# Optimization experiments

Measured on AMD Instinct MI355X. Metric: run time of the kernel, lower is better.

Reference implementation:

```python
import jax, jax.numpy as jnp
import numpy as np

B, C = 4096, 10000
TAU = 1.0
MIN_K, MAX_K = 30, 100


def setup_inputs() -> dict:
    key = jax.random.key(0)
    k1, k2 = jax.random.split(key, 2)
    logit = jax.random.normal(k1, (B, C), dtype=jnp.float32)
    target = jax.random.randint(k2, (B,), 0, C)
    # long-tailed class counts: exponential decay from 1000 down to 5
    cls_num = np.exp(np.linspace(np.log(1000.0), np.log(5.0), C)).astype(np.float32)
    cls_num_ratio = cls_num / cls_num.sum()
    log_cls_num = jnp.asarray(np.log(cls_num_ratio + 1e-6), dtype=jnp.float32)
    freq = (cls_num.max() / cls_num).astype(np.float32)
    freq_norm = (freq - freq.min()) / (freq.max() - freq.min() + 1e-6)
    k_per_class = jnp.asarray((freq_norm * (MAX_K - MIN_K) + MIN_K).astype(np.int32))
    return {"logit": logit, "target": target, "log_cls_num": log_cls_num,
            "k_per_class": k_per_class}


def reference(logit, target, log_cls_num, k_per_class):
    b, c = logit.shape
    rows = jnp.arange(b)
    # logit-adjusted cross entropy (loss_full)
    logit_adj = logit + TAU * log_cls_num[None, :]
    log_p_adj = jax.nn.log_softmax(logit_adj, axis=1)  # [B, C]
    loss_full = -jnp.mean(log_p_adj[rows, target])
    # per-row variable-k top-k mask on the ORIGINAL logits
    prob_adj = jnp.exp(log_p_adj)
    k = jnp.minimum(k_per_class[target], c)            # [B]
    sorted_desc = -jnp.sort(-logit, axis=1)            # [B, C] descending
    thresh = sorted_desc[rows, k - 1]                  # k-th largest per row
    mask = logit >= thresh[:, None]
    masked_prob = jnp.where(mask, prob_adj, 0.0) + 1e-6
    masked_prob = masked_prob / masked_prob.sum(axis=1, keepdims=True)
    loss_topk = -jnp.mean(jnp.log(masked_prob)[rows, target])
    return 0.5 * loss_full + 0.5 * loss_topk
```

## Files before the change

kernel.cpp:

```cpp
#include <hip/hip_runtime.h>

#define BLOCK 256
#define C_DIM 10000
#define C4 (C_DIM / 4)
#define NIT ((C4 + BLOCK - 1) / BLOCK)
#define TAU 1.0f
#define CAP 2048
#define PIV_HI 2.0f
#define PIV_LO 1.0f

__device__ __forceinline__ unsigned flip_key(float f) {
    unsigned u = __float_as_uint(f);
    return (u & 0x80000000u) ? ~u : (u | 0x80000000u);
}
__device__ __forceinline__ float unflip_key(unsigned k) {
    unsigned u = (k & 0x80000000u) ? (k & 0x7fffffffu) : ~k;
    return __uint_as_float(u);
}

__global__ void zero_out_kernel(float* out, int n) {
    int i = blockIdx.x * blockDim.x + threadIdx.x;
    if (i < n) out[i] = 0.f;
}

__device__ __forceinline__ void scan_pick(unsigned* hist, int shift, int tid,
                                          unsigned* shp, unsigned* shkr, unsigned* shcnt) {
    unsigned h0 = hist[4 * tid + 0], h1 = hist[4 * tid + 1];
    unsigned h2 = hist[4 * tid + 2], h3 = hist[4 * tid + 3];
    unsigned loc = h0 + h1 + h2 + h3;
    unsigned suf = loc;
    for (int off = 1; off < 64; off <<= 1) {
        unsigned o = __shfl_down(suf, off);
        if (tid + off < 64) suf += o;
    }
    unsigned sufex = suf - loc;
    unsigned kr = *shkr;
    unsigned s3 = sufex + h3;
    unsigned s2 = s3 + h2;
    unsigned s1 = s2 + h1;
    unsigned s0 = s1 + h0;
    int bsel = -1; unsigned newkr = 0, newcnt = 0;
    if      (s3 >= kr && s3 - h3 < kr) { bsel = 4 * tid + 3; newkr = kr - (s3 - h3); newcnt = h3; }
    else if (s2 >= kr && s2 - h2 < kr) { bsel = 4 * tid + 2; newkr = kr - (s2 - h2); newcnt = h2; }
    else if (s1 >= kr && s1 - h1 < kr) { bsel = 4 * tid + 1; newkr = kr - (s1 - h1); newcnt = h1; }
    else if (s0 >= kr && s0 - h0 < kr) { bsel = 4 * tid + 0; newkr = kr - (s0 - h0); newcnt = h0; }
    if (bsel >= 0) {
        *shp |= ((unsigned)bsel << shift);
        *shkr = newkr;
        *shcnt = newcnt;
    }
}

__global__ __launch_bounds__(BLOCK, 8) void topk_la_loss_kernel(
    const float* __restrict__ logit, const int* __restrict__ target,
    const float* __restrict__ lcn, const int* __restrict__ kpc,
    float* __restrict__ out, int B) {
    __shared__ unsigned hist[256];
    __shared__ unsigned candk[CAP];
    __shared__ unsigned short candi[CAP];
    __shared__ float red_a[4], red_b[4];
    __shared__ unsigned sh_nc, sh_prefix, sh_kr, sh_cnt;
    __shared__ int sh_path, sh_k;
    __shared__ float sh_thresh, sh_madj;

    const int row = blockIdx.x;
    const int tid = threadIdx.x;
    const int lane = tid & 63;
    const int wid = tid >> 6;
    const float* lrow = logit + (size_t)row * C_DIM;

    if (tid == 0) {
        int t = target[row];
        int k = kpc[t];
        if (k > C_DIM) k = C_DIM;
        sh_k = k;
        sh_nc = 0u;
    }
    __syncthreads();

    float z = 0.f, madj = -INFINITY;
    for (int it = 0; it < NIT; ++it) {
        int j4 = it * BLOCK + tid;
        if (j4 < C4) {
            float4 f = ((const float4*)lrow)[j4];
            float4 l = ((const float4*)lcn)[j4];
            float a0 = f.x + TAU * l.x, a1 = f.y + TAU * l.y;
            float a2 = f.z + TAU * l.z, a3 = f.w + TAU * l.w;
            z += __expf(a0) + __expf(a1) + __expf(a2) + __expf(a3);
            madj = fmaxf(madj, fmaxf(fmaxf(a0, a1), fmaxf(a2, a3)));
            int j = 4 * j4;
            if (f.x >= PIV_HI) { unsigned i = atomicAdd(&sh_nc, 1u); if (i < CAP) { candk[i] = __float_as_uint(f.x); candi[i] = (unsigned short)(j + 0); } }
            if (f.y >= PIV_HI) { unsigned i = atomicAdd(&sh_nc, 1u); if (i < CAP) { candk[i] = __float_as_uint(f.y); candi[i] = (unsigned short)(j + 1); } }
            if (f.z >= PIV_HI) { unsigned i = atomicAdd(&sh_nc, 1u); if (i < CAP) { candk[i] = __float_as_uint(f.z); candi[i] = (unsigned short)(j + 2); } }
            if (f.w >= PIV_HI) { unsigned i = atomicAdd(&sh_nc, 1u); if (i < CAP) { candk[i] = __float_as_uint(f.w); candi[i] = (unsigned short)(j + 3); } }
        }
    }
    for (int off = 32; off; off >>= 1) madj = fmaxf(madj, __shfl_down(madj, off));
    if (lane == 0) red_a[wid] = madj;
    __syncthreads();

    if (tid == 0) {
        sh_madj = fmaxf(fmaxf(red_a[0], red_a[1]), fmaxf(red_a[2], red_a[3]));
        unsigned n = sh_nc;
        unsigned k = (unsigned)sh_k;
        sh_path = (n >= k && n <= CAP) ? 0 : ((n < k) ? 1 : 2);
        sh_kr = k;
        sh_prefix = 0u;
        sh_cnt = n;
    }
    __syncthreads();

    if (sh_path == 1) {
        if (tid == 0) sh_nc = 0u;
        __syncthreads();
        for (int it = 0; it < NIT; ++it) {
            int j4 = it * BLOCK + tid;
            if (j4 < C4) {
                float4 f = ((const float4*)lrow)[j4];
                int j = 4 * j4;
                if (f.x >= PIV_LO) { unsigned i = atomicAdd(&sh_nc, 1u); if (i < CAP) { candk[i] = __float_as_uint(f.x); candi[i] = (unsigned short)(j + 0); } }
                if (f.y >= PIV_LO) { unsigned i = atomicAdd(&sh_nc, 1u); if (i < CAP) { candk[i] = __float_as_uint(f.y); candi[i] = (unsigned short)(j + 1); } }
                if (f.z >= PIV_LO) { unsigned i = atomicAdd(&sh_nc, 1u); if (i < CAP) { candk[i] = __float_as_uint(f.z); candi[i] = (unsigned short)(j + 2); } }
                if (f.w >= PIV_LO) { unsigned i = atomicAdd(&sh_nc, 1u); if (i < CAP) { candk[i] = __float_as_uint(f.w); candi[i] = (unsigned short)(j + 3); } }
            }
        }
        __syncthreads();
        if (tid == 0) {
            unsigned n = sh_nc;
            unsigned k = (unsigned)sh_k;
            sh_path = (n >= k && n <= CAP) ? 0 : 2;
            sh_kr = k;
            sh_prefix = 0u;
            sh_cnt = n;
        }
        __syncthreads();
    }

    const int path = sh_path;
    const float madjB = sh_madj;

    if (path == 0) {
        const int nc = (int)sh_cnt;
        unsigned kmask = 0u;
        for (int q = 0; q < 4; ++q) {
            if (sh_cnt == 1u) break;
            const int shift = 24 - 8 * q;
            hist[tid] = 0u;
            __syncthreads();
            const unsigned pref = sh_prefix;
            for (int i = tid; i < nc; i += BLOCK) {
                unsigned kk = candk[i];
                if ((kk & kmask) == pref) atomicAdd(&hist[(kk >> shift) & 0xFFu], 1u);
            }
            __syncthreads();
            if (tid < 64) scan_pick(hist, shift, tid, &sh_prefix, &sh_kr, &sh_cnt);
            kmask |= (0xFFu << shift);
            __syncthreads();
        }
        if (sh_cnt == 1u && kmask != 0xFFFFFFFFu) {
            const unsigned pref = sh_prefix;
            __syncthreads();
            for (int i = tid; i < nc; i += BLOCK) {
                unsigned kk = candk[i];
                if ((kk & kmask) == pref) sh_prefix = kk;
            }
            __syncthreads();
        }
        if (tid == 0) sh_thresh = __uint_as_float(sh_prefix);
    } else {
        for (int p = 0; p < 4; ++p) {
            const int shift = 24 - 8 * p;
            const unsigned pmask = p ? (0xFFFFFFFFu << (shift + 8)) : 0u;
            hist[tid] = 0u;
            __syncthreads();
            const unsigned pref = sh_prefix;
            for (int it = 0; it < NIT; ++it) {
                int j4 = it * BLOCK + tid;
                if (j4 < C4) {
                    float4 f = ((const float4*)lrow)[j4];
                    unsigned kk;
                    kk = flip_key(f.x); if ((kk & pmask) == pref) atomicAdd(&hist[(kk >> shift) & 0xFFu], 1u);
                    kk = flip_key(f.y); if ((kk & pmask) == pref) atomicAdd(&hist[(kk >> shift) & 0xFFu], 1u);
                    kk = flip_key(f.z); if ((kk & pmask) == pref) atomicAdd(&hist[(kk >> shift) & 0xFFu], 1u);
                    kk = flip_key(f.w); if ((kk & pmask) == pref) atomicAdd(&hist[(kk >> shift) & 0xFFu], 1u);
                }
            }
            __syncthreads();
            if (tid < 64) scan_pick(hist, shift, tid, &sh_prefix, &sh_kr, &sh_cnt);
            __syncthreads();
        }
        if (tid == 0) sh_thresh = unflip_key(sh_prefix);
    }
    __syncthreads();

    const float thresh = sh_thresh;
    const bool rare = fabsf(madjB) > 80.f;

    float sm = 0.f;
    if (!rare) {
        if (path == 0) {
            const int nc = (int)((sh_nc <= CAP) ? sh_nc : CAP);
            for (int i = tid; i < nc; i += BLOCK) {
                unsigned kk = candk[i];
                float v = __uint_as_float(kk);
                if (v >= thresh) sm += __expf(v + TAU * lcn[candi[i]]);
            }
        } else {
            for (int it = 0; it < NIT; ++it) {
                int j4 = it * BLOCK + tid;
                if (j4 < C4) {
                    float4 f = ((const float4*)lrow)[j4];
                    float4 l = ((const float4*)lcn)[j4];
                    if (f.x >= thresh) sm += __expf(f.x + TAU * l.x);
                    if (f.y >= thresh) sm += __expf(f.y + TAU * l.y);
                    if (f.z >= thresh) sm += __expf(f.z + TAU * l.z);
                    if (f.w >= thresh) sm += __expf(f.w + TAU * l.w);
                }
            }
        }
    } else {
        z = 0.f;
        for (int it = 0; it < NIT; ++it) {
            int j4 = it * BLOCK + tid;
            if (j4 < C4) {
                float4 f = ((const float4*)lrow)[j4];
                float4 l = ((const float4*)lcn)[j4];
                float e;
                e = __expf(f.x + TAU * l.x - madjB); z += e; if (f.x >= thresh) sm += e;
                e = __expf(f.y + TAU * l.y - madjB); z += e; if (f.y >= thresh) sm += e;
                e = __expf(f.z + TAU * l.z - madjB); z += e; if (f.z >= thresh) sm += e;
                e = __expf(f.w + TAU * l.w - madjB); z += e; if (f.w >= thresh) sm += e;
            }
        }
    }

    for (int off = 32; off; off >>= 1) {
        z  += __shfl_down(z, off);
        sm += __shfl_down(sm, off);
    }
    if (lane == 0) { red_a[wid] = z; red_b[wid] = sm; }
    __syncthreads();

    if (tid == 0) {
        float Z = red_a[0] + red_a[1] + red_a[2] + red_a[3];
        float S = red_b[0] + red_b[1] + red_b[2] + red_b[3];
        int t = target[row];
        float logit_t = lrow[t];
        float adj_t = logit_t + TAU * lcn[t];
        float sub = rare ? madjB : 0.f;
        float lpt = adj_t - sub - __logf(Z);
        float p_num = ((logit_t >= thresh) ? __expf(lpt) : 0.f) + 1e-6f;
        float Smask = S / Z + (float)C_DIM * 1e-6f;
        float loss = 0.5f * (-lpt + __logf(Smask) - __logf(p_num));
        atomicAdd(out, loss / (float)B);
    }
}

extern "C" void kernel_launch(void* const* d_in, const int* in_sizes, int n_in,
                              void* d_out, int out_size, void* d_ws, size_t ws_size,
                              hipStream_t stream) {
    const float* logit  = (const float*)d_in[0];
    const int*   target = (const int*)d_in[1];
    const float* lcn    = (const float*)d_in[2];
    const int*   kpc    = (const int*)d_in[3];
    float* out = (float*)d_out;
    const int B = in_sizes[1];

    zero_out_kernel<<<1, 64, 0, stream>>>(out, out_size);
    topk_la_loss_kernel<<<B, BLOCK, 0, stream>>>(logit, target, lcn, kpc, out, B);
}
```

Baseline: 270.5 us.

## Process one row per wavefront with ballot-based candidate compaction

Each 64-lane wavefront now handles a whole row, with four rows per block, instead of one row per 256-thread block. Block-wide __syncthreads and shared-memory reductions are replaced by wave shuffles, and the radix pick is done inside the wave. Shared atomic counters for candidate gathering give way to ballot/mbcnt prefix compaction, and the candidate buffer shrinks to 512 entries per wave. Each lane now walks more of the row, so per-row latency goes up. The smaller candidate cap also sends more rows to the full-row radix fallback when more than 512 values pass the pivot.

```diff
diff --git a/kernel.cpp b/kernel.cpp
--- a/kernel.cpp
+++ b/kernel.cpp
@@ -1,11 +1,12 @@
 #include <hip/hip_runtime.h>
 
 #define BLOCK 256
+#define WPB 4
 #define C_DIM 10000
 #define C4 (C_DIM / 4)
-#define NIT ((C4 + BLOCK - 1) / BLOCK)
+#define NIT4 ((C4 + 63) / 64)
 #define TAU 1.0f
-#define CAP 2048
+#define CAP 512
 #define PIV_HI 2.0f
 #define PIV_LO 1.0f
 
@@ -17,197 +18,190 @@
     unsigned u = (k & 0x80000000u) ? (k & 0x7fffffffu) : ~k;
     return __uint_as_float(u);
 }
+__device__ __forceinline__ int mbcnt64(unsigned long long m) {
+    return (int)__builtin_amdgcn_mbcnt_hi((unsigned)(m >> 32),
+               __builtin_amdgcn_mbcnt_lo((unsigned)(m & 0xffffffffu), 0u));
+}
 
 __global__ void zero_out_kernel(float* out, int n) {
     int i = blockIdx.x * blockDim.x + threadIdx.x;
     if (i < n) out[i] = 0.f;
 }
 
-__device__ __forceinline__ void scan_pick(unsigned* hist, int shift, int tid,
-                                          unsigned* shp, unsigned* shkr, unsigned* shcnt) {
-    unsigned h0 = hist[4 * tid + 0], h1 = hist[4 * tid + 1];
-    unsigned h2 = hist[4 * tid + 2], h3 = hist[4 * tid + 3];
-    unsigned loc = h0 + h1 + h2 + h3;
+__device__ __forceinline__ void wave_pick(uint4 hv, int lane, int shift,
+                                          unsigned& prefix, unsigned& kr, unsigned& cnt) {
+    unsigned loc = hv.x + hv.y + hv.z + hv.w;
     unsigned suf = loc;
+    #pragma unroll
     for (int off = 1; off < 64; off <<= 1) {
-        unsigned o = __shfl_down(suf, off);
-        if (tid + off < 64) suf += o;
+        unsigned o = (unsigned)__shfl_down((int)suf, off);
+        if (lane + off < 64) suf += o;
     }
     unsigned sufex = suf - loc;
-    unsigned kr = *shkr;
-    unsigned s3 = sufex + h3;
-    unsigned s2 = s3 + h2;
-    unsigned s1 = s2 + h1;
-    unsigned s0 = s1 + h0;
-    int bsel = -1; unsigned newkr = 0, newcnt = 0;
-    if      (s3 >= kr && s3 - h3 < kr) { bsel = 4 * tid + 3; newkr = kr - (s3 - h3); newcnt = h3; }
-    else if (s2 >= kr && s2 - h2 < kr) { bsel = 4 * tid + 2; newkr = kr - (s2 - h2); newcnt = h2; }
-    else if (s1 >= kr && s1 - h1 < kr) { bsel = 4 * tid + 1; newkr = kr - (s1 - h1); newcnt = h1; }
-    else if (s0 >= kr && s0 - h0 < kr) { bsel = 4 * tid + 0; newkr = kr - (s0 - h0); newcnt = h0; }
-    if (bsel >= 0) {
-        *shp |= ((unsigned)bsel << shift);
-        *shkr = newkr;
-        *shcnt = newcnt;
-    }
-}
-
-__global__ __launch_bounds__(BLOCK, 8) void topk_la_loss_kernel(
+    unsigned s3 = sufex + hv.w;
+    unsigned s2 = s3 + hv.z;
+    unsigned s1 = s2 + hv.y;
+    unsigned s0 = s1 + hv.x;
+    int bsel = -1; unsigned nkr = 0u, ncnt = 0u;
+    if      (s3 >= kr && s3 - hv.w < kr) { bsel = 4 * lane + 3; nkr = kr - (s3 - hv.w); ncnt = hv.w; }
+    else if (s2 >= kr && s2 - hv.z < kr) { bsel = 4 * lane + 2; nkr = kr - (s2 - hv.z); ncnt = hv.z; }
+    else if (s1 >= kr && s1 - hv.y < kr) { bsel = 4 * lane + 1; nkr = kr - (s1 - hv.y); ncnt = hv.y; }
+    else if (s0 >= kr && s0 - hv.x < kr) { bsel = 4 * lane + 0; nkr = kr - (s0 - hv.x); ncnt = hv.x; }
+    unsigned long long pm = __ballot(bsel >= 0);
+    int src = __ffsll((unsigned long long)pm) - 1;
+    prefix |= ((unsigned)__shfl(bsel, src)) << shift;
+    kr  = (unsigned)__shfl((int)nkr, src);
+    cnt = (unsigned)__shfl((int)ncnt, src);
+}
+
+__global__ __launch_bounds__(BLOCK, 4) void topk_la_loss_kernel(
     const float* __restrict__ logit, const int* __restrict__ target,
     const float* __restrict__ lcn, const int* __restrict__ kpc,
     float* __restrict__ out, int B) {
-    __shared__ unsigned hist[256];
-    __shared__ unsigned candk[CAP];
-    __shared__ unsigned short candi[CAP];
-    __shared__ float red_a[4], red_b[4];
-    __shared__ unsigned sh_nc, sh_prefix, sh_kr, sh_cnt;
-    __shared__ int sh_path, sh_k;
-    __shared__ float sh_thresh, sh_madj;
-
-    const int row = blockIdx.x;
+    __shared__ unsigned candk[WPB][CAP];
+    __shared__ unsigned short candi[WPB][CAP];
+    __shared__ unsigned hist[WPB][256];
+
     const int tid = threadIdx.x;
     const int lane = tid & 63;
     const int wid = tid >> 6;
+    const int row = blockIdx.x * WPB + wid;
+    if (row >= B) return;
+
     const float* lrow = logit + (size_t)row * C_DIM;
-
-    if (tid == 0) {
-        int t = target[row];
-        int k = kpc[t];
-        if (k > C_DIM) k = C_DIM;
-        sh_k = k;
-        sh_nc = 0u;
-    }
-    __syncthreads();
-
-    float z = 0.f, madj = -INFINITY;
-    for (int it = 0; it < NIT; ++it) {
-        int j4 = it * BLOCK + tid;
+    unsigned* ck = candk[wid];
+    unsigned short* ci = candi[wid];
+    unsigned* h = hist[wid];
+
+    const int t = target[row];
+    int k = kpc[t]; if (k > C_DIM) k = C_DIM;
+
+    float z = 0.f, madj = -__builtin_inff();
+    unsigned nb = 0u;
+    #pragma unroll 2
+    for (int it = 0; it < NIT4; ++it) {
+        const int j4 = it * 64 + lane;
+        float4 f, l;
         if (j4 < C4) {
-            float4 f = ((const float4*)lrow)[j4];
-            float4 l = ((const float4*)lcn)[j4];
-            float a0 = f.x + TAU * l.x, a1 = f.y + TAU * l.y;
-            float a2 = f.z + TAU * l.z, a3 = f.w + TAU * l.w;
-            z += __expf(a0) + __expf(a1) + __expf(a2) + __expf(a3);
-            madj = fmaxf(madj, fmaxf(fmaxf(a0, a1), fmaxf(a2, a3)));
-            int j = 4 * j4;
-            if (f.x >= PIV_HI) { unsigned i = atomicAdd(&sh_nc, 1u); if (i < CAP) { candk[i] = __float_as_uint(f.x); candi[i] = (unsigned short)(j + 0); } }
-            if (f.y >= PIV_HI) { unsigned i = atomicAdd(&sh_nc, 1u); if (i < CAP) { candk[i] = __float_as_uint(f.y); candi[i] = (unsigned short)(j + 1); } }
-            if (f.z >= PIV_HI) { unsigned i = atomicAdd(&sh_nc, 1u); if (i < CAP) { candk[i] = __float_as_uint(f.z); candi[i] = (unsigned short)(j + 2); } }
-            if (f.w >= PIV_HI) { unsigned i = atomicAdd(&sh_nc, 1u); if (i < CAP) { candk[i] = __float_as_uint(f.w); candi[i] = (unsigned short)(j + 3); } }
-        }
-    }
-    for (int off = 32; off; off >>= 1) madj = fmaxf(madj, __shfl_down(madj, off));
-    if (lane == 0) red_a[wid] = madj;
-    __syncthreads();
-
-    if (tid == 0) {
-        sh_madj = fmaxf(fmaxf(red_a[0], red_a[1]), fmaxf(red_a[2], red_a[3]));
-        unsigned n = sh_nc;
-        unsigned k = (unsigned)sh_k;
-        sh_path = (n >= k && n <= CAP) ? 0 : ((n < k) ? 1 : 2);
-        sh_kr = k;
-        sh_prefix = 0u;
-        sh_cnt = n;
-    }
-    __syncthreads();
-
-    if (sh_path == 1) {
-        if (tid == 0) sh_nc = 0u;
-        __syncthreads();
-        for (int it = 0; it < NIT; ++it) {
-            int j4 = it * BLOCK + tid;
-            if (j4 < C4) {
-                float4 f = ((const float4*)lrow)[j4];
-                int j = 4 * j4;
-                if (f.x >= PIV_LO) { unsigned i = atomicAdd(&sh_nc, 1u); if (i < CAP) { candk[i] = __float_as_uint(f.x); candi[i] = (unsigned short)(j + 0); } }
-                if (f.y >= PIV_LO) { unsigned i = atomicAdd(&sh_nc, 1u); if (i < CAP) { candk[i] = __float_as_uint(f.y); candi[i] = (unsigned short)(j + 1); } }
-                if (f.z >= PIV_LO) { unsigned i = atomicAdd(&sh_nc, 1u); if (i < CAP) { candk[i] = __float_as_uint(f.z); candi[i] = (unsigned short)(j + 2); } }
-                if (f.w >= PIV_LO) { unsigned i = atomicAdd(&sh_nc, 1u); if (i < CAP) { candk[i] = __float_as_uint(f.w); candi[i] = (unsigned short)(j + 3); } }
-            }
-        }
-        __syncthreads();
-        if (tid == 0) {
-            unsigned n = sh_nc;
-            unsigned k = (unsigned)sh_k;
-            sh_path = (n >= k && n <= CAP) ? 0 : 2;
-            sh_kr = k;
-            sh_prefix = 0u;
-            sh_cnt = n;
-        }
-        __syncthreads();
-    }
-
-    const int path = sh_path;
-    const float madjB = sh_madj;
-
+            f = ((const float4*)lrow)[j4];
+            l = ((const float4*)lcn)[j4];
+        } else {
+            f = make_float4(-1e30f, -1e30f, -1e30f, -1e30f);
+            l = make_float4(0.f, 0.f, 0.f, 0.f);
+        }
+        const float a0 = f.x + TAU * l.x, a1 = f.y + TAU * l.y;
+        const float a2 = f.z + TAU * l.z, a3 = f.w + TAU * l.w;
+        z += __expf(a0) + __expf(a1) + __expf(a2) + __expf(a3);
+        madj = fmaxf(madj, fmaxf(fmaxf(a0, a1), fmaxf(a2, a3)));
+        const int j = 4 * j4;
+        unsigned long long m;
+        m = __ballot(f.x >= PIV_HI);
+        if (f.x >= PIV_HI) { unsigned p = nb + (unsigned)mbcnt64(m); if (p < CAP) { ck[p] = __float_as_uint(f.x); ci[p] = (unsigned short)(j + 0); } }
+        nb += (unsigned)__popcll(m);
+        m = __ballot(f.y >= PIV_HI);
+        if (f.y >= PIV_HI) { unsigned p = nb + (unsigned)mbcnt64(m); if (p < CAP) { ck[p] = __float_as_uint(f.y); ci[p] = (unsigned short)(j + 1); } }
+        nb += (unsigned)__popcll(m);
+        m = __ballot(f.z >= PIV_HI);
+        if (f.z >= PIV_HI) { unsigned p = nb + (unsigned)mbcnt64(m); if (p < CAP) { ck[p] = __float_as_uint(f.z); ci[p] = (unsigned short)(j + 2); } }
+        nb += (unsigned)__popcll(m);
+        m = __ballot(f.w >= PIV_HI);
+        if (f.w >= PIV_HI) { unsigned p = nb + (unsigned)mbcnt64(m); if (p < CAP) { ck[p] = __float_as_uint(f.w); ci[p] = (unsigned short)(j + 3); } }
+        nb += (unsigned)__popcll(m);
+    }
+    #pragma unroll
+    for (int off = 32; off; off >>= 1) madj = fmaxf(madj, __shfl_xor(madj, off));
+
+    unsigned n = nb;
+    int path = (n >= (unsigned)k && n <= CAP) ? 0 : ((n < (unsigned)k) ? 1 : 2);
+
+    if (path == 1) {
+        nb = 0u;
+        for (int it = 0; it < NIT4; ++it) {
+            const int j4 = it * 64 + lane;
+            float4 f;
+            if (j4 < C4) f = ((const float4*)lrow)[j4];
+            else f = make_float4(-1e30f, -1e30f, -1e30f, -1e30f);
+            const int j = 4 * j4;
+            unsigned long long m;
+            m = __ballot(f.x >= PIV_LO);
+            if (f.x >= PIV_LO) { unsigned p = nb + (unsigned)mbcnt64(m); if (p < CAP) { ck[p] = __float_as_uint(f.x); ci[p] = (unsigned short)(j + 0); } }
+            nb += (unsigned)__popcll(m);
+            m = __ballot(f.y >= PIV_LO);
+            if (f.y >= PIV_LO) { unsigned p = nb + (unsigned)mbcnt64(m); if (p < CAP) { ck[p] = __float_as_uint(f.y); ci[p] = (unsigned short)(j + 1); } }
+            nb += (unsigned)__popcll(m);
+            m = __ballot(f.z >= PIV_LO);
+            if (f.z >= PIV_LO) { unsigned p = nb + (unsigned)mbcnt64(m); if (p < CAP) { ck[p] = __float_as_uint(f.z); ci[p] = (unsigned short)(j + 2); } }
+            nb += (unsigned)__popcll(m);
+            m = __ballot(f.w >= PIV_LO);
+            if (f.w >= PIV_LO) { unsigned p = nb + (unsigned)mbcnt64(m); if (p < CAP) { ck[p] = __float_as_uint(f.w); ci[p] = (unsigned short)(j + 3); } }
+            nb += (unsigned)__popcll(m);
+        }
+        n = nb;
+        path = (n >= (unsigned)k && n <= CAP) ? 0 : 2;
+    }
+
+    float thresh;
     if (path == 0) {
-        const int nc = (int)sh_cnt;
-        unsigned kmask = 0u;
+        const int nc = (int)n;
+        unsigned prefix = 0u, kr = (unsigned)k, cnt = n, kmask = 0u;
         for (int q = 0; q < 4; ++q) {
-            if (sh_cnt == 1u) break;
+            if (cnt == 1u) break;
             const int shift = 24 - 8 * q;
-            hist[tid] = 0u;
-            __syncthreads();
-            const unsigned pref = sh_prefix;
-            for (int i = tid; i < nc; i += BLOCK) {
-                unsigned kk = candk[i];
-                if ((kk & kmask) == pref) atomicAdd(&hist[(kk >> shift) & 0xFFu], 1u);
-            }
-            __syncthreads();
-            if (tid < 64) scan_pick(hist, shift, tid, &sh_prefix, &sh_kr, &sh_cnt);
+            *(uint4*)&h[4 * lane] = make_uint4(0u, 0u, 0u, 0u);
+            for (int i = lane; i < nc; i += 64) {
+                unsigned kk = ck[i];
+                if ((kk & kmask) == prefix) atomicAdd(&h[(kk >> shift) & 0xFFu], 1u);
+            }
+            uint4 hv = *(const uint4*)&h[4 * lane];
+            wave_pick(hv, lane, shift, prefix, kr, cnt);
             kmask |= (0xFFu << shift);
-            __syncthreads();
-        }
-        if (sh_cnt == 1u && kmask != 0xFFFFFFFFu) {
-            const unsigned pref = sh_prefix;
-            __syncthreads();
-            for (int i = tid; i < nc; i += BLOCK) {
-                unsigned kk = candk[i];
-                if ((kk & kmask) == pref) sh_prefix = kk;
-            }
-            __syncthreads();
-        }
-        if (tid == 0) sh_thresh = __uint_as_float(sh_prefix);
+        }
+        if (cnt == 1u && kmask != 0xFFFFFFFFu) {
+            unsigned found = 0u;
+            for (int i = lane; i < nc; i += 64) {
+                unsigned kk = ck[i];
+                if ((kk & kmask) == prefix) found = kk;
+            }
+            #pragma unroll
+            for (int off = 32; off; off >>= 1) found |= (unsigned)__shfl_xor((int)found, off);
+            prefix = found;
+        }
+        thresh = __uint_as_float(prefix);
     } else {
+        unsigned prefix = 0u, kr = (unsigned)k, cnt = 0u;
         for (int p = 0; p < 4; ++p) {
             const int shift = 24 - 8 * p;
             const unsigned pmask = p ? (0xFFFFFFFFu << (shift + 8)) : 0u;
-            hist[tid] = 0u;
-            __syncthreads();
-            const unsigned pref = sh_prefix;
-            for (int it = 0; it < NIT; ++it) {
-                int j4 = it * BLOCK + tid;
+            *(uint4*)&h[4 * lane] = make_uint4(0u, 0u, 0u, 0u);
+            for (int it = 0; it < NIT4; ++it) {
+                const int j4 = it * 64 + lane;
                 if (j4 < C4) {
                     float4 f = ((const float4*)lrow)[j4];
                     unsigned kk;
-                    kk = flip_key(f.x); if ((kk & pmask) == pref) atomicAdd(&hist[(kk >> shift) & 0xFFu], 1u);
-                    kk = flip_key(f.y); if ((kk & pmask) == pref) atomicAdd(&hist[(kk >> shift) & 0xFFu], 1u);
-                    kk = flip_key(f.z); if ((kk & pmask) == pref) atomicAdd(&hist[(kk >> shift) & 0xFFu], 1u);
-                    kk = flip_key(f.w); if ((kk & pmask) == pref) atomicAdd(&hist[(kk >> shift) & 0xFFu], 1u);
+                    kk = flip_key(f.x); if ((kk & pmask) == prefix) atomicAdd(&h[(kk >> shift) & 0xFFu], 1u);
+                    kk = flip_key(f.y); if ((kk & pmask) == prefix) atomicAdd(&h[(kk >> shift) & 0xFFu], 1u);
+                    kk = flip_key(f.z); if ((kk & pmask) == prefix) atomicAdd(&h[(kk >> shift) & 0xFFu], 1u);
+                    kk = flip_key(f.w); if ((kk & pmask) == prefix) atomicAdd(&h[(kk >> shift) & 0xFFu], 1u);
                 }
             }
-            __syncthreads();
-            if (tid < 64) scan_pick(hist, shift, tid, &sh_prefix, &sh_kr, &sh_cnt);
-            __syncthreads();
-        }
-        if (tid == 0) sh_thresh = unflip_key(sh_prefix);
-    }
-    __syncthreads();
-
-    const float thresh = sh_thresh;
-    const bool rare = fabsf(madjB) > 80.f;
-
+            uint4 hv = *(const uint4*)&h[4 * lane];
+            wave_pick(hv, lane, shift, prefix, kr, cnt);
+        }
+        thresh = unflip_key(prefix);
+    }
+
+    const bool rare = fabsf(madj) > 80.f;
     float sm = 0.f;
     if (!rare) {
         if (path == 0) {
-            const int nc = (int)((sh_nc <= CAP) ? sh_nc : CAP);
-            for (int i = tid; i < nc; i += BLOCK) {
-                unsigned kk = candk[i];
-                float v = __uint_as_float(kk);
-                if (v >= thresh) sm += __expf(v + TAU * lcn[candi[i]]);
+            const int nc = (int)n;
+            for (int i = lane; i < nc; i += 64) {
+                const float v = __uint_as_float(ck[i]);
+                if (v >= thresh) sm += __expf(v + TAU * lcn[ci[i]]);
             }
         } else {
-            for (int it = 0; it < NIT; ++it) {
-                int j4 = it * BLOCK + tid;
+            for (int it = 0; it < NIT4; ++it) {
+                const int j4 = it * 64 + lane;
                 if (j4 < C4) {
                     float4 f = ((const float4*)lrow)[j4];
                     float4 l = ((const float4*)lcn)[j4];
@@ -220,38 +214,34 @@
         }
     } else {
         z = 0.f;
-        for (int it = 0; it < NIT; ++it) {
-            int j4 = it * BLOCK + tid;
+        for (int it = 0; it < NIT4; ++it) {
+            const int j4 = it * 64 + lane;
             if (j4 < C4) {
                 float4 f = ((const float4*)lrow)[j4];
                 float4 l = ((const float4*)lcn)[j4];
                 float e;
-                e = __expf(f.x + TAU * l.x - madjB); z += e; if (f.x >= thresh) sm += e;
-                e = __expf(f.y + TAU * l.y - madjB); z += e; if (f.y >= thresh) sm += e;
-                e = __expf(f.z + TAU * l.z - madjB); z += e; if (f.z >= thresh) sm += e;
-                e = __expf(f.w + TAU * l.w - madjB); z += e; if (f.w >= thresh) sm += e;
-            }
-        }
-    }
-
+                e = __expf(f.x + TAU * l.x - madj); z += e; if (f.x >= thresh) sm += e;
+                e = __expf(f.y + TAU * l.y - madj); z += e; if (f.y >= thresh) sm += e;
+                e = __expf(f.z + TAU * l.z - madj); z += e; if (f.z >= thresh) sm += e;
+                e = __expf(f.w + TAU * l.w - madj); z += e; if (f.w >= thresh) sm += e;
+            }
+        }
+    }
+
+    #pragma unroll
     for (int off = 32; off; off >>= 1) {
         z  += __shfl_down(z, off);
         sm += __shfl_down(sm, off);
     }
-    if (lane == 0) { red_a[wid] = z; red_b[wid] = sm; }
-    __syncthreads();
-
-    if (tid == 0) {
-        float Z = red_a[0] + red_a[1] + red_a[2] + red_a[3];
-        float S = red_b[0] + red_b[1] + red_b[2] + red_b[3];
-        int t = target[row];
-        float logit_t = lrow[t];
-        float adj_t = logit_t + TAU * lcn[t];
-        float sub = rare ? madjB : 0.f;
-        float lpt = adj_t - sub - __logf(Z);
-        float p_num = ((logit_t >= thresh) ? __expf(lpt) : 0.f) + 1e-6f;
-        float Smask = S / Z + (float)C_DIM * 1e-6f;
-        float loss = 0.5f * (-lpt + __logf(Smask) - __logf(p_num));
+    if (lane == 0) {
+        const float Z = z, S = sm;
+        const float logit_t = lrow[t];
+        const float adj_t = logit_t + TAU * lcn[t];
+        const float sub = rare ? madj : 0.f;
+        const float lpt = adj_t - sub - __logf(Z);
+        const float p_num = ((logit_t >= thresh) ? __expf(lpt) : 0.f) + 1e-6f;
+        const float Smask = S / Z + (float)C_DIM * 1e-6f;
+        const float loss = 0.5f * (-lpt + __logf(Smask) - __logf(p_num));
         atomicAdd(out, loss / (float)B);
     }
 }
@@ -267,5 +257,6 @@
     const int B = in_sizes[1];
 
     zero_out_kernel<<<1, 64, 0, stream>>>(out, out_size);
-    topk_la_loss_kernel<<<B, BLOCK, 0, stream>>>(logit, target, lcn, kpc, out, B);
-}
+    const int nblk = (B + WPB - 1) / WPB;
+    topk_la_loss_kernel<<<nblk, BLOCK, 0, stream>>>(logit, target, lcn, kpc, out, B);
+}
```

Result: slower. 286.7 us (+6.0%).
